# Performance work log

Measured on AMD Instinct MI355X. Metric: run time of the kernel, lower is better.

The kernel has to match this reference:

```python
import jax, jax.numpy as jnp
import numpy as np


def normalize_adj(adj):
    """Symmetrize (adj + adj.T*(adj.T>adj) - adj*(adj.T>adj)), add self loops, row-normalize D^-1 A."""
    at = jnp.swapaxes(adj, -1, -2)
    mask = (at > adj).astype(adj.dtype)
    a = adj + at * mask - adj * mask
    m = a.shape[-1]
    a = a + jnp.eye(m, dtype=a.dtype)
    rowsum = a.sum(axis=-1, keepdims=True)
    inv = jnp.where(rowsum > 0, 1.0 / rowsum, 0.0)
    return a * inv


def setup_inputs() -> dict:
    key = jax.random.key(0)
    ks = jax.random.split(key, 8)
    N, n, T, dim, M = 4, 3, 512, 2048, 256
    x = jax.random.normal(ks[0], (N, n, T, dim), dtype=jnp.float32)
    nodes = jax.random.normal(ks[1], (N, M, dim), dtype=jnp.float32)
    adj = (jax.random.uniform(ks[2], (N, M, M)) < 0.05).astype(jnp.float32)
    conv_w = jax.random.normal(ks[3], (2048, dim, 3), dtype=jnp.float32) * 0.02  # OIH
    conv_b = jnp.zeros((2048,), dtype=jnp.float32)
    W1 = jax.random.normal(ks[4], (dim, dim), dtype=jnp.float32) * 0.02
    b1 = jnp.zeros((dim,), dtype=jnp.float32)
    W2 = jax.random.normal(ks[5], (dim, dim), dtype=jnp.float32) * 0.02
    b2 = jnp.zeros((dim,), dtype=jnp.float32)
    return {"x": x, "nodes": nodes, "adj": adj, "conv_w": conv_w, "conv_b": conv_b,
            "W1": W1, "b1": b1, "W2": W2, "b2": b2}


def reference(x, nodes, adj, conv_w, conv_b, W1, b1, W2, b2):
    N, n, T, dim = x.shape
    # Conv1d front-end: (N*n, C=dim, T), kernel 3, pad 1, then ReLU
    feats = x.reshape(N * n, T, dim).transpose(0, 2, 1)  # [B, C, T]
    feats = jax.lax.conv_general_dilated(
        feats, conv_w, window_strides=(1,), padding=[(1, 1)],
        dimension_numbers=("NCH", "OIH", "NCH"))
    feats = jax.nn.relu(feats + conv_b[None, :, None])
    feats = feats.transpose(0, 2, 1).reshape(N, n, T, dim)
    # GCN_Module over per-sample node graphs (batched over N)
    a = normalize_adj(adj)                                   # [N, M, M]
    h = jax.nn.relu(jnp.einsum("bij,bjf->bif", a, nodes @ W1) + b1)
    out = jnp.einsum("bij,bjf->bif", a, h @ W2) + b2         # [N, M, dim]
    return feats, out
```

## Files before the change

### kernel.cpp

```cpp
#include <hip/hip_runtime.h>
#include <stdint.h>

typedef __bf16 bf16x8 __attribute__((ext_vector_type(8)));
typedef float floatx4 __attribute__((ext_vector_type(4)));

__device__ __forceinline__ void gload_lds16(const void* g, void* l) {
    __builtin_amdgcn_global_load_lds((const __attribute__((address_space(1))) void*)g,
                                     (__attribute__((address_space(3))) void*)l, 16, 0, 0);
}

__device__ __forceinline__ uint16_t f2bf(float f) {
    uint32_t u = __float_as_uint(f);
    u += 0x7fff + ((u >> 16) & 1);
    return (uint16_t)(u >> 16);
}
__device__ __forceinline__ uint32_t f2bf2(float lo, float hi) {
    return (uint32_t)f2bf(lo) | ((uint32_t)f2bf(hi) << 16);
}

struct AmulSM {
    float vv[256];
    int   jj[256];
    float part[4];
    int   wcnt[4];
    int   woff[4];
    float sinv;
    int   n0;
};

__device__ __forceinline__ void amul_body(const float* __restrict__ adj,
                                          const float* __restrict__ H,
                                          uint16_t* __restrict__ outp,
                                          int b, int i, int tid, AmulSM* sm)
{
    const float* A = adj + ((size_t)b << 16);
    float aij = A[(i << 8) + tid];
    float aji = A[(tid << 8) + i];
    float v = fmaxf(aij, aji);
    if (tid == i) v += 1.0f;

    float s = v;
    #pragma unroll
    for (int off = 32; off > 0; off >>= 1) s += __shfl_down(s, off);

    bool pred = v != 0.0f;
    unsigned long long m = __ballot(pred);
    int wid = tid >> 6;
    if ((tid & 63) == 0) { sm->part[wid] = s; sm->wcnt[wid] = (int)__popcll(m); }
    __syncthreads();
    if (tid == 0) {
        float t = sm->part[0] + sm->part[1] + sm->part[2] + sm->part[3];
        sm->sinv = t > 0.0f ? 1.0f / t : 0.0f;
        int o = 0;
        #pragma unroll
        for (int w = 0; w < 4; ++w) { sm->woff[w] = o; o += sm->wcnt[w]; }
        sm->n0 = o;
    }
    __syncthreads();
    if (pred) {
        int pos = sm->woff[wid] + (int)__popcll(m & ((1ull << (tid & 63)) - 1ull));
        sm->vv[pos] = v * sm->sinv;
        sm->jj[pos] = tid;
    }
    __syncthreads();

    const int n0 = sm->n0;
    const int f0 = tid * 8;
    const float* Hb = H + (((size_t)b) << 8) * 2048;
    float acc[8] = {};
    for (int c = 0; c < n0; ++c) {
        float av = sm->vv[c];
        const float* hp = Hb + (size_t)sm->jj[c] * 2048 + f0;
        float4 p = *(const float4*)hp;
        float4 q = *(const float4*)(hp + 4);
        acc[0] += av * p.x; acc[1] += av * p.y; acc[2] += av * p.z; acc[3] += av * p.w;
        acc[4] += av * q.x; acc[5] += av * q.y; acc[6] += av * q.z; acc[7] += av * q.w;
    }
    uint4 o;
    o.x = f2bf2(acc[0], acc[1]);
    o.y = f2bf2(acc[2], acc[3]);
    o.z = f2bf2(acc[4], acc[5]);
    o.w = f2bf2(acc[6], acc[7]);
    *(uint4*)(outp + (((size_t)b << 8) + i) * 2048 + f0) = o;
}

__device__ __forceinline__ void amul_swizzle(int bid, int& b, int& i) {
    int x = bid & 7, g = bid >> 3;
    b = x >> 1;
    i = ((x & 1) << 7) + g;
}

#define PR_AM 1024
#define PR_W  3072
#define PR_T  5120
#define PR_N  17456

__global__ __launch_bounds__(256)
void k_prep(const float* __restrict__ x, uint16_t* __restrict__ xpad,
            const float* __restrict__ w, uint16_t* __restrict__ wT,
            const float* __restrict__ W1, const float* __restrict__ W2,
            uint16_t* __restrict__ W1T, uint16_t* __restrict__ W2T,
            const float* __restrict__ adj, const float* __restrict__ nodes,
            uint16_t* __restrict__ gbf)
{
    __shared__ union {
        float  wbuf[6144];
        float  tile[64][65];
        AmulSM am;
    } sm;
    const int bid = blockIdx.x;
    const int tid = threadIdx.x;

    if (bid < PR_AM) {
        int b, i; amul_swizzle(bid, b, i);
        amul_body(adj, nodes, gbf, b, i, tid, &sm.am);
    } else if (bid < PR_W) {
        int o = bid - PR_AM;
        const float* src = w + (size_t)o * 6144;
        uint16_t*    dst = wT + (size_t)o * 6144;
        #pragma unroll
        for (int it = 0; it < 24; ++it)
            sm.wbuf[it * 256 + tid] = src[it * 256 + tid];
        __syncthreads();
        #pragma unroll
        for (int h = 0; h < 3; ++h)
            #pragma unroll
            for (int c = 0; c < 8; ++c) {
                int i = c * 256 + tid;
                dst[h * 2048 + i] = f2bf(sm.wbuf[i * 3 + h]);
            }
    } else if (bid < PR_T) {
        int t  = bid - PR_W;
        int z  = t >> 10;
        int by = (t >> 5) & 31;
        int bx = t & 31;
        const float* src = z ? W2 : W1;
        uint16_t*    dst = z ? W2T : W1T;
        int tx = tid & 63, ty = tid >> 6;
        for (int rr = ty; rr < 64; rr += 4)
            sm.tile[rr][tx] = src[(size_t)(by * 64 + rr) * 2048 + bx * 64 + tx];
        __syncthreads();
        for (int rr = ty; rr < 64; rr += 4)
            dst[(size_t)(bx * 64 + rr) * 2048 + by * 64 + tx] = f2bf(sm.tile[tx][rr]);
    } else {
        int idx4 = (bid - PR_T) * 256 + tid;
        int ch4  = idx4 & 511;
        int tmp  = idx4 >> 9;
        int b    = tmp / 514;
        int tt   = tmp - b * 514;
        float4 v = {0.0f, 0.0f, 0.0f, 0.0f};
        if (tt >= 1 && tt <= 512)
            v = *(const float4*)(x + ((size_t)(b * 512 + tt - 1) << 11) + ch4 * 4);
        uint2 o = { f2bf2(v.x, v.y), f2bf2(v.z, v.w) };
        ((uint2*)xpad)[idx4] = o;
    }
}

template<bool RELU>
__device__ __forceinline__ void g64_tile(uint16_t* As, uint16_t* Bs,
                                         const uint16_t* __restrict__ A,
                                         const uint16_t* __restrict__ BT,
                                         float* __restrict__ C, const float* __restrict__ bias,
                                         int rt, int ct, int tid)
{
    const int lane = tid & 63;
    const int wave = tid >> 6;
    const int wm   = (wave >> 1) * 32;
    const int wn   = (wave & 1) * 32;
    const int lm   = lane & 15;
    const int kq   = (lane >> 4) * 8;
    const int sr   = tid >> 2;
    const int sc   = (tid & 3) * 8;

    const size_t abase = (size_t)(rt + sr) * 2048 + sc;
    const size_t bbase = (size_t)(ct + sr) * 2048 + sc;

    floatx4 acc[2][2] = {};

    for (int k0 = 0; k0 < 2048; k0 += 64) {
        #pragma unroll
        for (int p = 0; p < 2; ++p) {
            gload_lds16(A  + abase + k0 + p * 32, &As[p * 2048 + tid * 8]);
            gload_lds16(BT + bbase + k0 + p * 32, &Bs[p * 2048 + tid * 8]);
        }
        __syncthreads();

        #pragma unroll
        for (int s = 0; s < 2; ++s) {
            bf16x8 af[2], bfr[2];
            #pragma unroll
            for (int mt = 0; mt < 2; ++mt)
                af[mt] = *(const bf16x8*)&As[s * 2048 + (wm + mt * 16 + lm) * 32 + kq];
            #pragma unroll
            for (int nt = 0; nt < 2; ++nt)
                bfr[nt] = *(const bf16x8*)&Bs[s * 2048 + (wn + nt * 16 + lm) * 32 + kq];
            #pragma unroll
            for (int mt = 0; mt < 2; ++mt)
                #pragma unroll
                for (int nt = 0; nt < 2; ++nt)
                    acc[mt][nt] = __builtin_amdgcn_mfma_f32_16x16x32_bf16(af[mt], bfr[nt], acc[mt][nt], 0, 0, 0);
        }
        __syncthreads();
    }

    const int lq = lane >> 4;
    #pragma unroll
    for (int mt = 0; mt < 2; ++mt)
        #pragma unroll
        for (int nt = 0; nt < 2; ++nt) {
            int col = ct + wn + nt * 16 + lm;
            float bv = bias[col];
            #pragma unroll
            for (int r = 0; r < 4; ++r) {
                int row = rt + wm + mt * 16 + lq * 4 + r;
                float v = acc[mt][nt][r] + bv;
                if (RELU) v = fmaxf(v, 0.0f);
                C[(size_t)row * 2048 + col] = v;
            }
        }
}

template<int BUF, bool STG, int VN>
__device__ __forceinline__ void conv_win(char* ldsb, int tid,
    const uint16_t*& aS0, const uint16_t*& aS1,
    const uint16_t*& bS0, const uint16_t*& bS1,
    int aoff, int boff, floatx4 (&acc)[6][4])
{
    char* As  = ldsb + BUF * 12288;
    char* Bs  = ldsb + 49152 + BUF * 16384;
    constexpr int NB = (BUF + 3) & 3;
    char* As3 = ldsb + NB * 12288;
    char* Bs3 = ldsb + 49152 + NB * 16384;

    bf16x8 av[3], bv[4];
    #pragma unroll
    for (int j = 0; j < 3; ++j) av[j] = *(const bf16x8*)(As + aoff + j * 1024);
    #pragma unroll
    for (int j = 0; j < 4; ++j) bv[j] = *(const bf16x8*)(Bs + boff + j * 1024);
    if constexpr (STG) {
        gload_lds16(aS0, As3 + tid * 16); aS0 += 32;
        if (tid < 256) { gload_lds16(aS1, As3 + 8192 + tid * 16); aS1 += 32; }
    }
    __builtin_amdgcn_s_barrier();
    asm volatile("s_waitcnt lgkmcnt(0)");
    __builtin_amdgcn_s_setprio(1);
    #pragma unroll
    for (int jm = 0; jm < 3; ++jm)
        #pragma unroll
        for (int fn = 0; fn < 4; ++fn)
            acc[jm][fn] = __builtin_amdgcn_mfma_f32_16x16x32_bf16(av[jm], bv[fn], acc[jm][fn], 0, 0, 0);
    __builtin_amdgcn_s_setprio(0);
    __builtin_amdgcn_s_barrier();
    #pragma unroll
    for (int j = 0; j < 3; ++j) av[j] = *(const bf16x8*)(As + aoff + 3072 + j * 1024);
    if constexpr (STG) {
        gload_lds16(bS0, Bs3 + tid * 16); bS0 += 32;
        gload_lds16(bS1, Bs3 + 8192 + tid * 16); bS1 += 32;
    }
    if constexpr (VN >= 0) asm volatile("s_waitcnt vmcnt(%0)" :: "i"(VN));
    __builtin_amdgcn_s_barrier();
    asm volatile("s_waitcnt lgkmcnt(0)");
    __builtin_amdgcn_s_setprio(1);
    #pragma unroll
    for (int jm = 0; jm < 3; ++jm)
        #pragma unroll
        for (int fn = 0; fn < 4; ++fn)
            acc[3 + jm][fn] = __builtin_amdgcn_mfma_f32_16x16x32_bf16(av[jm], bv[fn], acc[3 + jm][fn], 0, 0, 0);
    __builtin_amdgcn_s_setprio(0);
    __builtin_amdgcn_s_barrier();
}

__global__ __launch_bounds__(512, 2)
void k_big(const uint16_t* __restrict__ xpad, const uint16_t* __restrict__ wmT,
           float* __restrict__ feats, const float* __restrict__ conv_b,
           const uint16_t* __restrict__ gbf, const uint16_t* __restrict__ W1T,
           float* __restrict__ h, const float* __restrict__ b1)
{
    __shared__ __align__(16) char smem[114688];
    const int bid = blockIdx.x;
    const int tid = threadIdx.x;

    if (bid < 256) {
        const int xcd  = bid & 7;
        const int gg   = bid >> 3;
        const int tile = xcd * 32 + gg;
        const int rt   = (tile >> 3) * 192;
        const int ct   = (tile & 7) * 256;

        const int lane = tid & 63, wave = tid >> 6;
        const int mw = wave >> 2, nw = wave & 3;
        const int lm = lane & 15;
        const int kq2 = (lane >> 4) * 16;
        const int xc  = kq2 ^ ((lm & 3) << 4);
        const int aoff = ((mw * 96 + lm) << 6) + xc;
        const int boff = ((nw * 64 + lm) << 6) + xc;

        const int c1  = 512 + tid;
        const int r0  = tid >> 2,  kc0 = ((tid & 3) ^ (r0 & 3)) * 8;
        const int r1  = c1 >> 2,   kc1 = ((c1 & 3) ^ (r1 & 3)) * 8;

        const int RA0 = rt + r0;
        const int RA1 = rt + r1;
        const uint16_t* aS0 = xpad + (((size_t)((RA0 >> 9) * 514 + (RA0 & 511))) << 11) + kc0;
        const uint16_t* aS1 = xpad + (((size_t)((RA1 >> 9) * 514 + (RA1 & 511))) << 11) + kc1;
        const uint16_t* bS0 = wmT + (size_t)(ct + r0) * 6144 + kc0;
        const uint16_t* bS1 = wmT + (size_t)(ct + r1) * 6144 + kc1;

        #pragma unroll
        for (int p = 0; p < 3; ++p) {
            char* As3 = smem + p * 12288;
            char* Bs3 = smem + 49152 + p * 16384;
            gload_lds16(aS0, As3 + tid * 16); aS0 += 32;
            if (tid < 256) { gload_lds16(aS1, As3 + 8192 + tid * 16); aS1 += 32; }
            gload_lds16(bS0, Bs3 + tid * 16); bS0 += 32;
            gload_lds16(bS1, Bs3 + 8192 + tid * 16); bS1 += 32;
        }
        asm volatile("s_waitcnt vmcnt(6)");
        __builtin_amdgcn_s_barrier();

        floatx4 acc[6][4] = {};
        #pragma unroll 1
        for (int it = 0; it < 47; ++it) {
            conv_win<0, true, 6>(smem, tid, aS0, aS1, bS0, bS1, aoff, boff, acc);
            conv_win<1, true, 6>(smem, tid, aS0, aS1, bS0, bS1, aoff, boff, acc);
            conv_win<2, true, 6>(smem, tid, aS0, aS1, bS0, bS1, aoff, boff, acc);
            conv_win<3, true, 6>(smem, tid, aS0, aS1, bS0, bS1, aoff, boff, acc);
        }
        conv_win<0, true,  6>(smem, tid, aS0, aS1, bS0, bS1, aoff, boff, acc);
        conv_win<1, false, 3>(smem, tid, aS0, aS1, bS0, bS1, aoff, boff, acc);
        conv_win<2, false, 0>(smem, tid, aS0, aS1, bS0, bS1, aoff, boff, acc);
        conv_win<3, false,-1>(smem, tid, aS0, aS1, bS0, bS1, aoff, boff, acc);

        const int lq = lane >> 4;
        #pragma unroll
        for (int fm = 0; fm < 6; ++fm)
            #pragma unroll
            for (int fn = 0; fn < 4; ++fn) {
                int col = ct + nw * 64 + fn * 16 + lm;
                float bb = conv_b[col];
                #pragma unroll
                for (int r = 0; r < 4; ++r) {
                    int row = rt + mw * 96 + fm * 16 + lq * 4 + r;
                    feats[(size_t)row * 2048 + col] = fmaxf(acc[fm][fn][r] + bb, 0.0f);
                }
            }
    } else {
        const int t    = bid - 256;
        const int half = tid >> 8;
        const int st   = t * 2 + half;
        const int rt   = (st & 15) * 64;
        const int ct   = (st >> 4) * 64;
        uint16_t* As = (uint16_t*)smem + half * 8192;
        g64_tile<true>(As, As + 4096, gbf, W1T, h, b1, rt, ct, tid & 255);
    }
}

__global__ __launch_bounds__(256)
void k_amul(const float* __restrict__ adj, const float* __restrict__ H,
            uint16_t* __restrict__ outp)
{
    __shared__ AmulSM sm;
    int b, i; amul_swizzle(blockIdx.x, b, i);
    amul_body(adj, H, outp, b, i, threadIdx.x, &sm);
}

__global__ __launch_bounds__(256)
void k_gemm64(const uint16_t* __restrict__ A, const uint16_t* __restrict__ BT,
              float* __restrict__ C, const float* __restrict__ bias)
{
    __shared__ __align__(16) uint16_t lds[8192];
    const int bid = blockIdx.x;
    const int xc  = bid & 7;
    const int g   = bid >> 3;
    const int rt  = (g & 15) * 64;
    const int ct  = (4 * xc + (g >> 4)) * 64;
    g64_tile<false>(lds, lds + 4096, A, BT, C, bias, rt, ct, threadIdx.x);
}


extern "C" void kernel_launch(void* const* d_in, const int* in_sizes, int n_in,
                              void* d_out, int out_size, void* d_ws, size_t ws_size,
                              hipStream_t stream)
{
    const float* x      = (const float*)d_in[0];
    const float* nodes  = (const float*)d_in[1];
    const float* adj    = (const float*)d_in[2];
    const float* conv_w = (const float*)d_in[3];
    const float* conv_b = (const float*)d_in[4];
    const float* W1     = (const float*)d_in[5];
    const float* b1     = (const float*)d_in[6];
    const float* W2     = (const float*)d_in[7];
    const float* b2     = (const float*)d_in[8];
    float* out = (float*)d_out;

    char* ws = (char*)d_ws;
    uint16_t* xpad   = (uint16_t*)(ws);
    uint16_t* wmT    = (uint16_t*)(ws + 25288704);
    uint16_t* W1T    = (uint16_t*)(ws + 50454528);
    uint16_t* W2T    = (uint16_t*)(ws + 58843136);
    uint16_t* gbf    = (uint16_t*)(ws + 67231744);
    float*    h      = (float*)   (ws + 71426048);
    uint16_t* ahb    = (uint16_t*)(ws + 79814656);

    k_prep<<<PR_N, 256, 0, stream>>>(x, xpad, conv_w, wmT,
                                     W1, W2, W1T, W2T, adj, nodes, gbf);
    k_big<<<512, 512, 0, stream>>>(xpad, wmT, out, conv_b, gbf, W1T, h, b1);
    k_amul<<<1024, 256, 0, stream>>>(adj, h, ahb);
    k_gemm64<<<512, 256, 0, stream>>>(ahb, W2T, out + 12582912, b2);
}
```

Before: 389.2 us.

## Restructure conv GEMM mainloop to double-buffered BK=64 stages with new swizzle

Replaces the 4-stage ring of 32-wide K slices with a 2-stage double buffer of 64-wide K slices. Each stage issues all global-to-LDS loads up front, then runs four MFMA phases. It waits for the next buffer with a full vmcnt(0) before the last phase. The LDS layout and XOR swizzle change to match 128-byte rows. This halves the number of window iterations and the barrier/loop overhead per K element, at the cost of a shallower prefetch depth that may expose more global-load latency.

```diff
diff --git a/kernel.cpp b/kernel.cpp
--- a/kernel.cpp
+++ b/kernel.cpp
@@ -220,54 +220,64 @@
         }
 }
 
-template<int BUF, bool STG, int VN>
-__device__ __forceinline__ void conv_win(char* ldsb, int tid,
-    const uint16_t*& aS0, const uint16_t*& aS1,
-    const uint16_t*& bS0, const uint16_t*& bS1,
-    int aoff, int boff, floatx4 (&acc)[6][4])
-{
-    char* As  = ldsb + BUF * 12288;
-    char* Bs  = ldsb + 49152 + BUF * 16384;
-    constexpr int NB = (BUF + 3) & 3;
-    char* As3 = ldsb + NB * 12288;
-    char* Bs3 = ldsb + 49152 + NB * 16384;
+template<int CUR, bool STG>
+__device__ __forceinline__ void conv_win64(char* smemb, int tid,
+    const uint16_t* (&aP)[3], const uint16_t* (&bP)[4],
+    int abase, int bbase, floatx4 (&acc)[6][4])
+{
+    char* As  = smemb + CUR * 24576;
+    char* Bs  = smemb + 49152 + CUR * 32768;
+    char* Asn = smemb + (CUR ^ 1) * 24576;
+    char* Bsn = smemb + 49152 + (CUR ^ 1) * 32768;
+
+    if constexpr (STG) {
+        gload_lds16(aP[0], Asn + tid * 16);
+        gload_lds16(aP[1], Asn + tid * 16 + 8192);
+        gload_lds16(aP[2], Asn + tid * 16 + 16384);
+        gload_lds16(bP[0], Bsn + tid * 16);
+        gload_lds16(bP[1], Bsn + tid * 16 + 8192);
+        gload_lds16(bP[2], Bsn + tid * 16 + 16384);
+        gload_lds16(bP[3], Bsn + tid * 16 + 24576);
+        #pragma unroll
+        for (int j = 0; j < 3; ++j) aP[j] += 64;
+        #pragma unroll
+        for (int j = 0; j < 4; ++j) bP[j] += 64;
+    }
 
     bf16x8 av[3], bv[4];
-    #pragma unroll
-    for (int j = 0; j < 3; ++j) av[j] = *(const bf16x8*)(As + aoff + j * 1024);
-    #pragma unroll
-    for (int j = 0; j < 4; ++j) bv[j] = *(const bf16x8*)(Bs + boff + j * 1024);
-    if constexpr (STG) {
-        gload_lds16(aS0, As3 + tid * 16); aS0 += 32;
-        if (tid < 256) { gload_lds16(aS1, As3 + 8192 + tid * 16); aS1 += 32; }
-    }
+
+#define CONV_PHASE(ACCBASE)                                                   \
+    __builtin_amdgcn_s_barrier();                                             \
+    asm volatile("s_waitcnt lgkmcnt(0)");                                     \
+    __builtin_amdgcn_s_setprio(1);                                            \
+    _Pragma("unroll")                                                         \
+    for (int j = 0; j < 3; ++j)                                               \
+        _Pragma("unroll")                                                     \
+        for (int nf = 0; nf < 4; ++nf)                                        \
+            acc[ACCBASE + j][nf] = __builtin_amdgcn_mfma_f32_16x16x32_bf16(   \
+                av[j], bv[nf], acc[ACCBASE + j][nf], 0, 0, 0);                \
+    __builtin_amdgcn_s_setprio(0);                                            \
     __builtin_amdgcn_s_barrier();
-    asm volatile("s_waitcnt lgkmcnt(0)");
-    __builtin_amdgcn_s_setprio(1);
-    #pragma unroll
-    for (int jm = 0; jm < 3; ++jm)
-        #pragma unroll
-        for (int fn = 0; fn < 4; ++fn)
-            acc[jm][fn] = __builtin_amdgcn_mfma_f32_16x16x32_bf16(av[jm], bv[fn], acc[jm][fn], 0, 0, 0);
-    __builtin_amdgcn_s_setprio(0);
-    __builtin_amdgcn_s_barrier();
-    #pragma unroll
-    for (int j = 0; j < 3; ++j) av[j] = *(const bf16x8*)(As + aoff + 3072 + j * 1024);
-    if constexpr (STG) {
-        gload_lds16(bS0, Bs3 + tid * 16); bS0 += 32;
-        gload_lds16(bS1, Bs3 + 8192 + tid * 16); bS1 += 32;
-    }
-    if constexpr (VN >= 0) asm volatile("s_waitcnt vmcnt(%0)" :: "i"(VN));
-    __builtin_amdgcn_s_barrier();
-    asm volatile("s_waitcnt lgkmcnt(0)");
-    __builtin_amdgcn_s_setprio(1);
-    #pragma unroll
-    for (int jm = 0; jm < 3; ++jm)
-        #pragma unroll
-        for (int fn = 0; fn < 4; ++fn)
-            acc[3 + jm][fn] = __builtin_amdgcn_mfma_f32_16x16x32_bf16(av[jm], bv[fn], acc[3 + jm][fn], 0, 0, 0);
-    __builtin_amdgcn_s_setprio(0);
-    __builtin_amdgcn_s_barrier();
+
+    #pragma unroll
+    for (int nf = 0; nf < 4; ++nf) bv[nf] = *(const bf16x8*)(Bs + bbase + nf * 2048);
+    #pragma unroll
+    for (int j = 0; j < 3; ++j)  av[j]  = *(const bf16x8*)(As + abase + j * 2048);
+    CONV_PHASE(0)
+    #pragma unroll
+    for (int j = 0; j < 3; ++j)  av[j]  = *(const bf16x8*)(As + abase + 6144 + j * 2048);
+    CONV_PHASE(3)
+    #pragma unroll
+    for (int nf = 0; nf < 4; ++nf) bv[nf] = *(const bf16x8*)(Bs + bbase + 64 + nf * 2048);
+    #pragma unroll
+    for (int j = 0; j < 3; ++j)  av[j]  = *(const bf16x8*)(As + abase + 64 + j * 2048);
+    CONV_PHASE(0)
+    #pragma unroll
+    for (int j = 0; j < 3; ++j)  av[j]  = *(const bf16x8*)(As + abase + 6144 + 64 + j * 2048);
+    if constexpr (STG) asm volatile("s_waitcnt vmcnt(0)");
+    CONV_PHASE(3)
+
+#undef CONV_PHASE
 }
 
 __global__ __launch_bounds__(512, 2)
@@ -289,49 +299,57 @@
 
         const int lane = tid & 63, wave = tid >> 6;
         const int mw = wave >> 2, nw = wave & 3;
-        const int lm = lane & 15;
-        const int kq2 = (lane >> 4) * 16;
-        const int xc  = kq2 ^ ((lm & 3) << 4);
-        const int aoff = ((mw * 96 + lm) << 6) + xc;
-        const int boff = ((nw * 64 + lm) << 6) + xc;
-
-        const int c1  = 512 + tid;
-        const int r0  = tid >> 2,  kc0 = ((tid & 3) ^ (r0 & 3)) * 8;
-        const int r1  = c1 >> 2,   kc1 = ((c1 & 3) ^ (r1 & 3)) * 8;
-
-        const int RA0 = rt + r0;
-        const int RA1 = rt + r1;
-        const uint16_t* aS0 = xpad + (((size_t)((RA0 >> 9) * 514 + (RA0 & 511))) << 11) + kc0;
-        const uint16_t* aS1 = xpad + (((size_t)((RA1 >> 9) * 514 + (RA1 & 511))) << 11) + kc1;
-        const uint16_t* bS0 = wmT + (size_t)(ct + r0) * 6144 + kc0;
-        const uint16_t* bS1 = wmT + (size_t)(ct + r1) * 6144 + kc1;
-
-        #pragma unroll
-        for (int p = 0; p < 3; ++p) {
-            char* As3 = smem + p * 12288;
-            char* Bs3 = smem + 49152 + p * 16384;
-            gload_lds16(aS0, As3 + tid * 16); aS0 += 32;
-            if (tid < 256) { gload_lds16(aS1, As3 + 8192 + tid * 16); aS1 += 32; }
-            gload_lds16(bS0, Bs3 + tid * 16); bS0 += 32;
-            gload_lds16(bS1, Bs3 + 8192 + tid * 16); bS1 += 32;
-        }
-        asm volatile("s_waitcnt vmcnt(6)");
-        __builtin_amdgcn_s_barrier();
+        const int lm = lane & 15, lq = lane >> 4;
+        const int xorv  = (lm & 4) << 3;
+        const int abase = (mw * 96 + lm) * 128 + ((lq * 16) ^ xorv);
+        const int bbase = (nw * 64 + lm) * 128 + ((lq * 16) ^ xorv);
+
+        const uint16_t* aP[3];
+        const uint16_t* bP[4];
+        #pragma unroll
+        for (int j = 0; j < 3; ++j) {
+            int p   = tid + 512 * j;
+            int row = p >> 3;
+            int ls  = (p & 7) ^ (((p >> 5) & 1) << 1);
+            int R   = rt + row;
+            aP[j] = xpad + (((size_t)((R >> 9) * 514 + (R & 511))) << 11) + ls * 8;
+        }
+        #pragma unroll
+        for (int j = 0; j < 4; ++j) {
+            int p   = tid + 512 * j;
+            int row = p >> 3;
+            int ls  = (p & 7) ^ (((p >> 5) & 1) << 1);
+            bP[j] = wmT + (size_t)(ct + row) * 6144 + ls * 8;
+        }
+
+        {
+            char* As0 = smem;
+            char* Bs0 = smem + 49152;
+            gload_lds16(aP[0], As0 + tid * 16);
+            gload_lds16(aP[1], As0 + tid * 16 + 8192);
+            gload_lds16(aP[2], As0 + tid * 16 + 16384);
+            gload_lds16(bP[0], Bs0 + tid * 16);
+            gload_lds16(bP[1], Bs0 + tid * 16 + 8192);
+            gload_lds16(bP[2], Bs0 + tid * 16 + 16384);
+            gload_lds16(bP[3], Bs0 + tid * 16 + 24576);
+            #pragma unroll
+            for (int j = 0; j < 3; ++j) aP[j] += 64;
+            #pragma unroll
+            for (int j = 0; j < 4; ++j) bP[j] += 64;
+            asm volatile("s_waitcnt vmcnt(0)");
+            __builtin_amdgcn_s_barrier();
+        }
 
         floatx4 acc[6][4] = {};
         #pragma unroll 1
         for (int it = 0; it < 47; ++it) {
-            conv_win<0, true, 6>(smem, tid, aS0, aS1, bS0, bS1, aoff, boff, acc);
-            conv_win<1, true, 6>(smem, tid, aS0, aS1, bS0, bS1, aoff, boff, acc);
-            conv_win<2, true, 6>(smem, tid, aS0, aS1, bS0, bS1, aoff, boff, acc);
-            conv_win<3, true, 6>(smem, tid, aS0, aS1, bS0, bS1, aoff, boff, acc);
-        }
-        conv_win<0, true,  6>(smem, tid, aS0, aS1, bS0, bS1, aoff, boff, acc);
-        conv_win<1, false, 3>(smem, tid, aS0, aS1, bS0, bS1, aoff, boff, acc);
-        conv_win<2, false, 0>(smem, tid, aS0, aS1, bS0, bS1, aoff, boff, acc);
-        conv_win<3, false,-1>(smem, tid, aS0, aS1, bS0, bS1, aoff, boff, acc);
-
-        const int lq = lane >> 4;
+            conv_win64<0, true>(smem, tid, aP, bP, abase, bbase, acc);
+            conv_win64<1, true>(smem, tid, aP, bP, abase, bbase, acc);
+        }
+        conv_win64<0, true >(smem, tid, aP, bP, abase, bbase, acc);
+        conv_win64<1, false>(smem, tid, aP, bP, abase, bbase, acc);
+
+        const int lqe = lane >> 4;
         #pragma unroll
         for (int fm = 0; fm < 6; ++fm)
             #pragma unroll
@@ -340,7 +358,7 @@
                 float bb = conv_b[col];
                 #pragma unroll
                 for (int r = 0; r < 4; ++r) {
-                    int row = rt + mw * 96 + fm * 16 + lq * 4 + r;
+                    int row = rt + mw * 96 + fm * 16 + lqe * 4 + r;
                     feats[(size_t)row * 2048 + col] = fmaxf(acc[fm][fn][r] + bb, 0.0f);
                 }
             }
```

Result: no change. 394.0 us (+1.2%).
